# Performance work log

Measured on AMD Instinct MI355X. Metric: run time of the kernel, lower is better.

## Reference

```python
import jax, jax.numpy as jnp
import numpy as np

B, T, H = 2, 2048, 1024
NUM_HEADS = 16
HEAD_DIM = H // NUM_HEADS
MAX_REL = 4


def setup_inputs() -> dict:
    key = jax.random.key(0)
    ks = jax.random.split(key, 12)
    s = 1.0 / np.sqrt(H)
    inp = {
        "x": jax.random.normal(ks[0], (B, T, H), dtype=jnp.float32),
        "text_mask": jax.random.randint(ks[1], (B, T), 0, 2, dtype=jnp.int32),
        "Wq": jax.random.normal(ks[2], (H, H), dtype=jnp.float32) * s,
        "bq": jnp.zeros((H,), dtype=jnp.float32),
        "Wk": jax.random.normal(ks[3], (H, H), dtype=jnp.float32) * s,
        "bk": jnp.zeros((H,), dtype=jnp.float32),
        "Wv": jax.random.normal(ks[4], (H, H), dtype=jnp.float32) * s,
        "bv": jnp.zeros((H,), dtype=jnp.float32),
        "Wo": jax.random.normal(ks[5], (H, H), dtype=jnp.float32) * s,
        "bo": jnp.zeros((H,), dtype=jnp.float32),
        "rel_bias": jax.random.normal(ks[6], (2 * MAX_REL + 1, NUM_HEADS), dtype=jnp.float32),
    }
    return inp


def reference(x, text_mask, Wq, bq, Wk, bk, Wv, bv, Wo, bo, rel_bias):
    b, t, h = x.shape
    scale = HEAD_DIM ** (-0.5)

    def proj(W, bias):
        # [b,t,h] -> [b,heads,t,head_dim]
        return (x @ W.T + bias).reshape(b, t, NUM_HEADS, HEAD_DIM).transpose(0, 2, 1, 3)

    q = proj(Wq, bq)
    k = proj(Wk, bk)
    v = proj(Wv, bv)

    scores = jnp.einsum("bhqd,bhkd->bhqk", q, k) * scale  # [b,heads,t,t]

    pos = jnp.arange(t)
    rel = jnp.clip(pos[None, :] - pos[:, None], -MAX_REL, MAX_REL) + MAX_REL  # [t,t]
    bias = rel_bias[rel]  # [t,t,heads]
    scores = scores + bias.transpose(2, 0, 1)[None]  # broadcast over batch

    key_valid = text_mask.astype(bool)  # [b,t]
    scores = jnp.where(key_valid[:, None, None, :], scores, -10000.0)

    attn = jax.nn.softmax(scores, axis=-1)
    hidden = jnp.einsum("bhqk,bhkd->bhqd", attn, v)
    hidden = hidden.transpose(0, 2, 1, 3).reshape(b, t, h)
    out = hidden @ Wo.T + bo
    return out * text_mask.astype(out.dtype)[:, :, None]
```

## Files before the change

### kernel.cpp

```cpp
#include <hip/hip_runtime.h>
#include <hip/hip_bf16.h>

#define B_ 2
#define T_ 2048
#define H_ 1024
#define NH 16
#define HD 64

typedef __attribute__((ext_vector_type(8))) short bf16x8;
typedef __attribute__((ext_vector_type(4))) short bf16x4;
typedef __attribute__((ext_vector_type(4))) float f32x4;

#define ASYNC_COPY16(gptr, lptr)                                              \
    __builtin_amdgcn_global_load_lds(                                         \
        (const __attribute__((address_space(1))) void*)(gptr),                \
        (__attribute__((address_space(3))) void*)(lptr), 16, 0, 0)

#if __has_builtin(__builtin_amdgcn_exp2f)
#define EXP2(x) __builtin_amdgcn_exp2f(x)
#else
static __device__ inline float EXP2(float x) {
    float r;
    asm volatile("v_exp_f32 %0, %1" : "=v"(r) : "v"(x));
    return r;
}
#endif

static __device__ inline unsigned short f2bf(float f) {
    union { float f; unsigned u; } v; v.f = f;
    unsigned r = v.u + 0x7fff + ((v.u >> 16) & 1);
    return (unsigned short)(r >> 16);
}

static __device__ inline unsigned pkbf(float a, float b) {
    float2 t2; t2.x = a; t2.y = b;
    __hip_bfloat162 h = __float22bfloat162_rn(t2);
    union { __hip_bfloat162 h; unsigned u; } cv; cv.h = h;
    return cv.u;
}

static __device__ inline bf16x4 mk4(unsigned lo, unsigned hi) {
    union { bf16x4 v; unsigned u[2]; } cv;
    cv.u[0] = lo; cv.u[1] = hi;
    return cv.v;
}

static __device__ inline f32x4 zero4() {
    f32x4 z = {0.f, 0.f, 0.f, 0.f};
    return z;
}

#define LOG2E 1.44269504088896f

__global__ void cvt_kernel(const float* __restrict__ x,
                           const float* __restrict__ wq,
                           const float* __restrict__ wk,
                           const float* __restrict__ wv,
                           const float* __restrict__ wo,
                           const int* __restrict__ maskp,
                           unsigned short* __restrict__ dst,
                           unsigned* __restrict__ cidx,
                           unsigned short* __restrict__ vidx,
                           unsigned short* __restrict__ maskc,
                           unsigned* __restrict__ meta,
                           float* __restrict__ outz) {
    if (blockIdx.x > 8192) {
        long long idx =
            ((long long)(blockIdx.x - 8193) * 256 + threadIdx.x) * 4;
        if (idx < 4194304LL) {
            float4 z = {0.f, 0.f, 0.f, 0.f};
            *(float4*)(outz + idx) = z;
        }
        return;
    }
    if (blockIdx.x == 8192) {
        __shared__ unsigned ps[256];
        int t = threadIdx.x;
        int base = t * 16;
        int bb = base >> 11;
        unsigned mv = 0, cnt = 0;
#pragma unroll
        for (int i = 0; i < 16; i++) {
            if (maskp[base + i]) { mv |= (1u << i); cnt++; }
        }
        ps[t] = cnt;
        __syncthreads();
        for (int off = 1; off < 128; off <<= 1) {
            unsigned add = ((t & 127) >= off) ? ps[t - off] : 0;
            __syncthreads();
            ps[t] += add;
            __syncthreads();
        }
        unsigned cnt0 = ps[127], cnt1 = ps[255];
        unsigned ex = ps[t] - cnt;
        unsigned local = ex;
        unsigned g = (bb ? cnt0 : 0) + ex;
        for (int i = 0; i < 16; i++) {
            if (mv & (1u << i)) {
                cidx[g] = (unsigned)(base + i);
                vidx[bb * 2048 + local] =
                    (unsigned short)(base + i - bb * 2048);
                maskc[bb * 2048 + local] = 0x3F80;
                g++; local++;
            }
        }
        if (t == 0) { meta[0] = cnt0; meta[1] = cnt1; meta[2] = cnt0 + cnt1; }
        __syncthreads();
        unsigned C = cnt0 + cnt1;
        for (unsigned i = C + t; i < 4224; i += 256) cidx[i] = 0;
        for (unsigned i = cnt0 + t; i < 2048; i += 256) {
            vidx[i] = 0; maskc[i] = 0;
        }
        for (unsigned i = cnt1 + t; i < 2048; i += 256) {
            vidx[2048 + i] = 0; maskc[2048 + i] = 0;
        }
        return;
    }
    long long i0 = ((long long)blockIdx.x * blockDim.x + threadIdx.x) * 4;
    const float* src; long long off;
    if (i0 < 4194304LL)      { src = x;  off = i0; }
    else if (i0 < 5242880LL) { src = wq; off = i0 - 4194304LL; }
    else if (i0 < 6291456LL) { src = wk; off = i0 - 5242880LL; }
    else if (i0 < 7340032LL) { src = wv; off = i0 - 6291456LL; }
    else                     { src = wo; off = i0 - 7340032LL; }
    float4 f = *(const float4*)(src + off);
    ushort4 o;
    o.x = f2bf(f.x); o.y = f2bf(f.y); o.z = f2bf(f.z); o.w = f2bf(f.w);
    *(ushort4*)(dst + i0) = o;
}

__global__ __launch_bounds__(256) void qkv_gemm(
    const unsigned short* __restrict__ A,
    const unsigned short* __restrict__ Bm,
    const float* __restrict__ bq, const float* __restrict__ bk,
    const float* __restrict__ bv,
    const unsigned* __restrict__ cidx, const unsigned* __restrict__ meta,
    unsigned short* __restrict__ qout, unsigned short* __restrict__ kout,
    unsigned short* __restrict__ vout) {
    const int K = 1024;
    int C  = (int)meta[2];
    int c0 = (int)meta[0];
    int m0 = blockIdx.y * 64, n0 = blockIdx.x * 128;
    if (m0 >= C) return;
    __shared__ __align__(16) unsigned short As[64 * 32];
    __shared__ __align__(16) unsigned short Bs[128 * 32];
    int t = threadIdx.x;
    int w = t >> 6, lane = t & 63;
    int wm = (w >> 1) * 32, wn = (w & 1) * 64;
    int c = lane & 15, qd = lane >> 4;

    f32x4 acc[2][4];
#pragma unroll
    for (int i = 0; i < 2; i++)
#pragma unroll
        for (int j = 0; j < 4; j++) acc[i][j] = zero4();

    int srow = t >> 2, sseg = (t & 3) * 8;
    int r1 = (int)cidx[m0 + srow];
    const unsigned short* ag1 = A + (long long)r1 * K + sseg;
    const unsigned short* bg1 = Bm + (long long)(n0 + srow) * K + sseg;
    const unsigned short* bg2 = bg1 + 64LL * K;
    unsigned short* la1 = As + t * 8;
    unsigned short* lb1 = Bs + t * 8;
    unsigned short* lb2 = Bs + (t + 256) * 8;

    for (int kk = 0; kk < K; kk += 32) {
        __syncthreads();
        ASYNC_COPY16(ag1 + kk, la1);
        ASYNC_COPY16(bg1 + kk, lb1);
        ASYNC_COPY16(bg2 + kk, lb2);
        __syncthreads();
        bf16x8 af[2], bf[4];
#pragma unroll
        for (int i = 0; i < 2; i++)
            af[i] = *(const bf16x8*)(As + (wm + i * 16 + c) * 32 + qd * 8);
#pragma unroll
        for (int j = 0; j < 4; j++)
            bf[j] = *(const bf16x8*)(Bs + (wn + j * 16 + c) * 32 + qd * 8);
#pragma unroll
        for (int i = 0; i < 2; i++)
#pragma unroll
            for (int j = 0; j < 4; j++)
                acc[i][j] = __builtin_amdgcn_mfma_f32_16x16x32_bf16(
                    af[i], bf[j], acc[i][j], 0, 0, 0);
    }

    int gr[2][4];
#pragma unroll
    for (int i = 0; i < 2; i++)
#pragma unroll
        for (int r = 0; r < 4; r++) {
            int m = m0 + wm + i * 16 + qd * 4 + r;
            gr[i][r] = (m < C) ? (int)cidx[m] : -1;
        }

    const float QSCALE = 0.125f * LOG2E;
#pragma unroll
    for (int i = 0; i < 2; i++) {
        int m_base = m0 + wm + i * 16 + qd * 4;
#pragma unroll
        for (int j = 0; j < 4; j++) {
            int n = n0 + wn + j * 16 + c;
            int sel = n >> 10, within = n & 1023;
            int head = within >> 6, d = within & 63;
            if (sel == 0) {
                float ba = bq[within];
#pragma unroll
                for (int r = 0; r < 4; r++) {
                    if (gr[i][r] >= 0) {
                        int bb = gr[i][r] >> 11;
                        int loc = (m_base + r) - (bb ? c0 : 0);
                        qout[(((long long)(bb * NH + head)) * T_ + loc) * HD +
                             d] = f2bf((acc[i][j][r] + ba) * QSCALE);
                    }
                }
            } else if (sel == 1) {
                float ba = bk[within];
#pragma unroll
                for (int r = 0; r < 4; r++) {
                    if (gr[i][r] >= 0) {
                        int bb = gr[i][r] >> 11;
                        int loc = (m_base + r) - (bb ? c0 : 0);
                        kout[(((long long)(bb * NH + head)) * T_ + loc) * HD +
                             d] = f2bf(acc[i][j][r] + ba);
                    }
                }
            } else {
                float ba = bv[within];
                int g0 = gr[i][0], g3 = gr[i][3];
                int bb0 = g0 >> 11;
                int loc0 = m_base - (bb0 ? c0 : 0);
                if (g3 >= 0 && bb0 == (g3 >> 11) && ((loc0 & 3) == 0)) {
                    uint2 ov;
                    ov.x = pkbf(acc[i][j][0] + ba, acc[i][j][1] + ba);
                    ov.y = pkbf(acc[i][j][2] + ba, acc[i][j][3] + ba);
                    *(uint2*)(vout +
                              (((long long)(bb0 * NH + head)) * HD + d) * T_ +
                              loc0) = ov;
                } else {
#pragma unroll
                    for (int r = 0; r < 4; r++) {
                        if (gr[i][r] >= 0) {
                            int bb = gr[i][r] >> 11;
                            int loc = (m_base + r) - (bb ? c0 : 0);
                            vout[(((long long)(bb * NH + head)) * HD + d) *
                                     T_ +
                                 loc] = f2bf(acc[i][j][r] + ba);
                        }
                    }
                }
            }
        }
    }
}

__global__ __launch_bounds__(256) void out_gemm(
    const unsigned short* __restrict__ A,
    const unsigned short* __restrict__ Bm,
    const float* __restrict__ bo,
    const unsigned* __restrict__ cidx, const unsigned* __restrict__ meta,
    float* __restrict__ out) {
    const int K = 1024;
    int C = (int)meta[2];
    int m0 = blockIdx.y * 64, n0 = blockIdx.x * 64;
    if (m0 >= C) return;
    __shared__ __align__(16) unsigned short As[64 * 32];
    __shared__ __align__(16) unsigned short Bs[64 * 32];
    int t = threadIdx.x;
    int w = t >> 6, lane = t & 63;
    int wm = (w >> 1) * 32, wn = (w & 1) * 32;
    int c = lane & 15, qd = lane >> 4;

    f32x4 acc[2][2];
#pragma unroll
    for (int i = 0; i < 2; i++)
#pragma unroll
        for (int j = 0; j < 2; j++) acc[i][j] = zero4();

    int srow = t >> 2, sseg = (t & 3) * 8;
    int r1 = (int)cidx[m0 + srow];
    const unsigned short* ag1 = A + (long long)r1 * K + sseg;
    const unsigned short* bg1 = Bm + (long long)(n0 + srow) * K + sseg;
    unsigned short* la1 = As + t * 8;
    unsigned short* lb1 = Bs + t * 8;

    for (int kk = 0; kk < K; kk += 32) {
        __syncthreads();
        ASYNC_COPY16(ag1 + kk, la1);
        ASYNC_COPY16(bg1 + kk, lb1);
        __syncthreads();
        bf16x8 af[2], bf[2];
#pragma unroll
        for (int i = 0; i < 2; i++)
            af[i] = *(const bf16x8*)(As + (wm + i * 16 + c) * 32 + qd * 8);
#pragma unroll
        for (int j = 0; j < 2; j++)
            bf[j] = *(const bf16x8*)(Bs + (wn + j * 16 + c) * 32 + qd * 8);
#pragma unroll
        for (int i = 0; i < 2; i++)
#pragma unroll
            for (int j = 0; j < 2; j++)
                acc[i][j] = __builtin_amdgcn_mfma_f32_16x16x32_bf16(
                    af[i], bf[j], acc[i][j], 0, 0, 0);
    }

#pragma unroll
    for (int i = 0; i < 2; i++) {
#pragma unroll
        for (int r = 0; r < 4; r++) {
            int m = m0 + wm + i * 16 + qd * 4 + r;
            if (m < C) {
                long long g = (long long)cidx[m];
#pragma unroll
                for (int j = 0; j < 2; j++) {
                    int n = n0 + wn + j * 16 + c;
                    out[g * 1024 + n] = acc[i][j][r] + bo[n];
                }
            }
        }
    }
}

__global__ __launch_bounds__(256, 2) void attn_kernel(
    const unsigned short* __restrict__ qg,
    const unsigned short* __restrict__ kg,
    const unsigned short* __restrict__ vTg,
    const float* __restrict__ rel_bias,
    const unsigned short* __restrict__ maskc,
    const unsigned short* __restrict__ vidxg,
    const unsigned* __restrict__ meta,
    unsigned short* __restrict__ hid) {
    int hb = blockIdx.x, qt = blockIdx.y;
    int h = hb & 15, b = hb >> 4;
    int cnt = (int)meta[b];
    if (qt * 128 >= cnt) return;
    int nkt = (cnt + 63) >> 6;
    int t = threadIdx.x, w = t >> 6, lane = t & 63;
    int c = lane & 15, qd = lane >> 4;

    __shared__ __align__(16) unsigned short lk[2][64 * 72];
    __shared__ __align__(16) unsigned short lvT[2][64 * 72];
    __shared__ __align__(16) unsigned short lmk[2][64];
    __shared__ __align__(16) unsigned short lki[2][64];
    __shared__ float lrbf[16];

    if (t < 9) lrbf[t] = rel_bias[t * 16 + h] * LOG2E;
    float rb0 = rel_bias[0 * 16 + h] * LOG2E;
    float rb8 = rel_bias[8 * 16 + h] * LOG2E;

    const unsigned short* qp =
        qg + (((long long)(b * NH + h)) * T_ + qt * 128) * HD;
    const unsigned short* kp = kg + ((long long)(b * NH + h)) * T_ * HD;
    const unsigned short* vp = vTg + ((long long)(b * NH + h)) * HD * T_;

    bf16x8 qf[2][2];
#pragma unroll
    for (int mt = 0; mt < 2; mt++)
#pragma unroll
        for (int ks = 0; ks < 2; ks++)
            qf[mt][ks] = *(const bf16x8*)(qp + (w * 32 + mt * 16 + c) * HD +
                                          ks * 32 + qd * 8);

    const int imin = qt * 128 + w * 32;
    int imin_t = (int)vidxg[b * 2048 + min(imin, cnt - 1)];
    int imax_t = (int)vidxg[b * 2048 + min(imin + 31, cnt - 1)];
    int itrue[2];
#pragma unroll
    for (int mt = 0; mt < 2; mt++)
        itrue[mt] =
            (int)vidxg[b * 2048 + min(imin + mt * 16 + c, cnt - 1)];

    f32x4 o[4][2];
    f32x4 lacc[2];
#pragma unroll
    for (int dt = 0; dt < 4; dt++)
#pragma unroll
        for (int mt = 0; mt < 2; mt++) o[dt][mt] = zero4();
    lacc[0] = zero4(); lacc[1] = zero4();

    int srow = t >> 2, sseg = (t & 3) * 16;
    const unsigned short* kst = kp + srow * HD + sseg;
    const unsigned short* vst = vp + srow * T_ + sseg;
    const unsigned short* mst = maskc + b * 2048 + t;
    const unsigned short* ist = vidxg + b * 2048 + t * 8;

    uint4 rk0 = *(const uint4*)(kst);
    uint4 rk1 = *(const uint4*)(kst + 8);
    uint4 rv0 = *(const uint4*)(vst);
    uint4 rv1 = *(const uint4*)(vst + 8);
    unsigned short rm = (t < 64) ? *mst : 0;
    uint4 rki = {0, 0, 0, 0};
    if (t < 8) rki = *(const uint4*)(ist);

    for (int kt = 0; kt < nkt; kt++) {
        unsigned short* KB = lk[kt & 1];
        unsigned short* VB = lvT[kt & 1];
        unsigned short* MK = lmk[kt & 1];
        unsigned short* KI = lki[kt & 1];
        *(uint4*)(KB + srow * 72 + sseg)     = rk0;
        *(uint4*)(KB + srow * 72 + sseg + 8) = rk1;
        *(uint4*)(VB + srow * 72 + sseg)     = rv0;
        *(uint4*)(VB + srow * 72 + sseg + 8) = rv1;
        if (t < 64) MK[t] = rm;
        if (t < 8) *(uint4*)(KI + t * 8) = rki;
        {
            int ktn = (kt < nkt - 1) ? kt + 1 : nkt - 1;
            rk0 = *(const uint4*)(kst + ktn * 64 * HD);
            rk1 = *(const uint4*)(kst + ktn * 64 * HD + 8);
            rv0 = *(const uint4*)(vst + ktn * 64);
            rv1 = *(const uint4*)(vst + ktn * 64 + 8);
            if (t < 64) rm = mst[ktn * 64];
            if (t < 8) rki = *(const uint4*)(ist + ktn * 64);
        }
        __syncthreads();

        int j0 = kt * 64;
        int jlo_t = (int)KI[0];
        int jhi_t = (int)KI[min(63, cnt - 1 - j0)];
        bool far_lo = (jhi_t <= imin_t - 4);
        bool far_hi = (jlo_t >= imax_t + 4);
        float ub = far_lo ? rb0 : rb8;
        bool nearband = !(far_lo || far_hi);

#pragma unroll
        for (int jt = 0; jt < 4; jt++) {
            bf16x8 kf0 = *(const bf16x8*)(KB + (jt * 16 + c) * 72 + qd * 8);
            bf16x8 kf1 =
                *(const bf16x8*)(KB + (jt * 16 + c) * 72 + 32 + qd * 8);
            bf16x4 vld4 = *(const bf16x4*)(MK + jt * 16 + qd * 4);
            ushort4 kiv = *(const ushort4*)(KI + jt * 16 + qd * 4);
            bf16x4 vf[4];
#pragma unroll
            for (int dt = 0; dt < 4; dt++)
                vf[dt] = *(const bf16x4*)(VB + (dt * 16 + c) * 72 + jt * 16 +
                                          qd * 4);
#pragma unroll
            for (int mt = 0; mt < 2; mt++) {
                f32x4 acc = zero4();
                acc = __builtin_amdgcn_mfma_f32_16x16x32_bf16(kf0, qf[mt][0],
                                                              acc, 0, 0, 0);
                acc = __builtin_amdgcn_mfma_f32_16x16x32_bf16(kf1, qf[mt][1],
                                                              acc, 0, 0, 0);
                float p0, p1, p2, p3;
                if (nearband) {
                    int it = itrue[mt];
                    int r0 = (int)kiv.x - it;
                    r0 = r0 < -4 ? -4 : (r0 > 4 ? 4 : r0);
                    int r1 = (int)kiv.y - it;
                    r1 = r1 < -4 ? -4 : (r1 > 4 ? 4 : r1);
                    int r2 = (int)kiv.z - it;
                    r2 = r2 < -4 ? -4 : (r2 > 4 ? 4 : r2);
                    int r3 = (int)kiv.w - it;
                    r3 = r3 < -4 ? -4 : (r3 > 4 ? 4 : r3);
                    p0 = EXP2(acc[0] + lrbf[r0 + 4]);
                    p1 = EXP2(acc[1] + lrbf[r1 + 4]);
                    p2 = EXP2(acc[2] + lrbf[r2 + 4]);
                    p3 = EXP2(acc[3] + lrbf[r3 + 4]);
                } else {
                    p0 = EXP2(acc[0] + ub);
                    p1 = EXP2(acc[1] + ub);
                    p2 = EXP2(acc[2] + ub);
                    p3 = EXP2(acc[3] + ub);
                }
                bf16x4 pfrag = mk4(pkbf(p0, p1), pkbf(p2, p3));
                lacc[mt] = __builtin_amdgcn_mfma_f32_16x16x16bf16_1k(
                    vld4, pfrag, lacc[mt], 0, 0, 0);
#pragma unroll
                for (int dt = 0; dt < 4; dt++)
                    o[dt][mt] = __builtin_amdgcn_mfma_f32_16x16x16bf16_1k(
                        vf[dt], pfrag, o[dt][mt], 0, 0, 0);
            }
        }
    }

#pragma unroll
    for (int mt = 0; mt < 2; mt++) {
        int rc = imin + mt * 16 + c;
        if (rc < cnt) {
            float invl = 1.0f / lacc[mt][0];
            long long row = (long long)b * T_ + itrue[mt];
#pragma unroll
            for (int dt = 0; dt < 4; dt++) {
                uint2 ov;
                ov.x = pkbf(o[dt][mt][0] * invl, o[dt][mt][1] * invl);
                ov.y = pkbf(o[dt][mt][2] * invl, o[dt][mt][3] * invl);
                *(uint2*)(hid + row * H_ + h * HD + dt * 16 + qd * 4) = ov;
            }
        }
    }
}

extern "C" void kernel_launch(void* const* d_in, const int* in_sizes, int n_in,
                              void* d_out, int out_size, void* d_ws,
                              size_t ws_size, hipStream_t stream) {
    const float* x    = (const float*)d_in[0];
    const int* maskp  = (const int*)d_in[1];
    const float* Wq   = (const float*)d_in[2];
    const float* bq   = (const float*)d_in[3];
    const float* Wk   = (const float*)d_in[4];
    const float* bk   = (const float*)d_in[5];
    const float* Wv   = (const float*)d_in[6];
    const float* bv   = (const float*)d_in[7];
    const float* Wo   = (const float*)d_in[8];
    const float* bo   = (const float*)d_in[9];
    const float* rb   = (const float*)d_in[10];
    float* out        = (float*)d_out;

    unsigned short* ws = (unsigned short*)d_ws;
    unsigned short* xb    = ws;
    unsigned short* wqkv  = ws + 4194304LL;
    unsigned short* wo_b  = ws + 7340032LL;
    unsigned short* qb    = ws + 8388608LL;
    unsigned short* kb    = ws + 12582912LL;
    unsigned short* vTb   = ws + 16777216LL;
    unsigned short* hid   = ws + 20971520LL;
    unsigned* meta        = (unsigned*)(ws + 25165824LL);
    unsigned* cidx        = (unsigned*)(ws + 25165856LL);
    unsigned short* vidx  = ws + 25174304LL;
    unsigned short* maskc = ws + 25178400LL;

    cvt_kernel<<<12289, 256, 0, stream>>>(x, Wq, Wk, Wv, Wo, maskp, ws, cidx,
                                          vidx, maskc, meta, out);
    qkv_gemm<<<dim3(24, 64), 256, 0, stream>>>(xb, wqkv, bq, bk, bv, cidx,
                                               meta, qb, kb, vTb);
    attn_kernel<<<dim3(32, 16), 256, 0, stream>>>(qb, kb, vTb, rb, maskc,
                                                  vidx, meta, hid);
    out_gemm<<<dim3(16, 64), 256, 0, stream>>>(hid, wo_b, bo, cidx, meta,
                                               out);
}
```

Measured before the change: 181.9 us.

## Split attention key range across two wave groups per block and merge partials

Attention blocks grow to 512 threads split into two groups of four waves. Each group handles alternating 64-key tiles with its own double-buffered LDS, and the partial outputs and row sums are combined through LDS at the end. This doubles the waves working on each query tile, aiming for better latency hiding and occupancy on the compacted key loop. In exchange, LDS use per block doubles, each group refills its staging registers with an extra key tile (the clamped last one) that is never consumed, and the merge adds an extra reduction and barrier.

Result: no change. 185.0 us (+1.7%).

```diff
diff --git a/kernel.cpp b/kernel.cpp
--- a/kernel.cpp
+++ b/kernel.cpp
@@ -321,7 +321,7 @@
     }
 }
 
-__global__ __launch_bounds__(256, 2) void attn_kernel(
+__global__ __launch_bounds__(512, 2) void attn_kernel(
     const unsigned short* __restrict__ qg,
     const unsigned short* __restrict__ kg,
     const unsigned short* __restrict__ vTg,
@@ -335,13 +335,17 @@
     int cnt = (int)meta[b];
     if (qt * 128 >= cnt) return;
     int nkt = (cnt + 63) >> 6;
-    int t = threadIdx.x, w = t >> 6, lane = t & 63;
+    int t = threadIdx.x;
+    int g = t >> 8;
+    int tg = t & 255;
+    int w = tg >> 6;
+    int lane = t & 63;
     int c = lane & 15, qd = lane >> 4;
 
-    __shared__ __align__(16) unsigned short lk[2][64 * 72];
-    __shared__ __align__(16) unsigned short lvT[2][64 * 72];
-    __shared__ __align__(16) unsigned short lmk[2][64];
-    __shared__ __align__(16) unsigned short lki[2][64];
+    __shared__ __align__(16) unsigned short lk[2][2][64 * 72];
+    __shared__ __align__(16) unsigned short lvT[2][2][64 * 72];
+    __shared__ __align__(16) unsigned short lmk[2][2][64];
+    __shared__ __align__(16) unsigned short lki[2][2][64];
     __shared__ float lrbf[16];
 
     if (t < 9) lrbf[t] = rel_bias[t * 16 + h] * LOG2E;
@@ -378,43 +382,48 @@
         for (int mt = 0; mt < 2; mt++) o[dt][mt] = zero4();
     lacc[0] = zero4(); lacc[1] = zero4();
 
-    int srow = t >> 2, sseg = (t & 3) * 16;
+    int srow = tg >> 2, sseg = (tg & 3) * 16;
     const unsigned short* kst = kp + srow * HD + sseg;
     const unsigned short* vst = vp + srow * T_ + sseg;
-    const unsigned short* mst = maskc + b * 2048 + t;
-    const unsigned short* ist = vidxg + b * 2048 + t * 8;
-
-    uint4 rk0 = *(const uint4*)(kst);
-    uint4 rk1 = *(const uint4*)(kst + 8);
-    uint4 rv0 = *(const uint4*)(vst);
-    uint4 rv1 = *(const uint4*)(vst + 8);
-    unsigned short rm = (t < 64) ? *mst : 0;
+    const unsigned short* mst = maskc + b * 2048 + tg;
+    const unsigned short* ist = vidxg + b * 2048 + tg * 8;
+
+    int kt0 = min(g, nkt - 1);
+    uint4 rk0 = *(const uint4*)(kst + kt0 * 64 * HD);
+    uint4 rk1 = *(const uint4*)(kst + kt0 * 64 * HD + 8);
+    uint4 rv0 = *(const uint4*)(vst + kt0 * 64);
+    uint4 rv1 = *(const uint4*)(vst + kt0 * 64 + 8);
+    unsigned short rm = (tg < 64) ? mst[kt0 * 64] : 0;
     uint4 rki = {0, 0, 0, 0};
-    if (t < 8) rki = *(const uint4*)(ist);
-
-    for (int kt = 0; kt < nkt; kt++) {
-        unsigned short* KB = lk[kt & 1];
-        unsigned short* VB = lvT[kt & 1];
-        unsigned short* MK = lmk[kt & 1];
-        unsigned short* KI = lki[kt & 1];
+    if (tg < 8) rki = *(const uint4*)(ist + kt0 * 64);
+
+    int maxiter = (nkt + 1) >> 1;
+    for (int it = 0; it < maxiter; it++) {
+        int kta = g + 2 * it;
+        bool active = (kta < nkt);
+        unsigned short* KB = lk[g][it & 1];
+        unsigned short* VB = lvT[g][it & 1];
+        unsigned short* MK = lmk[g][it & 1];
+        unsigned short* KI = lki[g][it & 1];
         *(uint4*)(KB + srow * 72 + sseg)     = rk0;
         *(uint4*)(KB + srow * 72 + sseg + 8) = rk1;
         *(uint4*)(VB + srow * 72 + sseg)     = rv0;
         *(uint4*)(VB + srow * 72 + sseg + 8) = rv1;
-        if (t < 64) MK[t] = rm;
-        if (t < 8) *(uint4*)(KI + t * 8) = rki;
+        if (tg < 64) MK[tg] = rm;
+        if (tg < 8) *(uint4*)(KI + tg * 8) = rki;
         {
-            int ktn = (kt < nkt - 1) ? kt + 1 : nkt - 1;
+            int ktn = min(kta + 2, nkt - 1);
             rk0 = *(const uint4*)(kst + ktn * 64 * HD);
             rk1 = *(const uint4*)(kst + ktn * 64 * HD + 8);
             rv0 = *(const uint4*)(vst + ktn * 64);
             rv1 = *(const uint4*)(vst + ktn * 64 + 8);
-            if (t < 64) rm = mst[ktn * 64];
-            if (t < 8) rki = *(const uint4*)(ist + ktn * 64);
-        }
-        __syncthreads();
-
-        int j0 = kt * 64;
+            if (tg < 64) rm = mst[ktn * 64];
+            if (tg < 8) rki = *(const uint4*)(ist + ktn * 64);
+        }
+        __syncthreads();
+        if (!active) continue;
+
+        int j0 = kta * 64;
         int jlo_t = (int)KI[0];
         int jhi_t = (int)KI[min(63, cnt - 1 - j0)];
         bool far_lo = (jhi_t <= imin_t - 4);
@@ -443,14 +452,14 @@
                                                               acc, 0, 0, 0);
                 float p0, p1, p2, p3;
                 if (nearband) {
-                    int it = itrue[mt];
-                    int r0 = (int)kiv.x - it;
+                    int itq = itrue[mt];
+                    int r0 = (int)kiv.x - itq;
                     r0 = r0 < -4 ? -4 : (r0 > 4 ? 4 : r0);
-                    int r1 = (int)kiv.y - it;
+                    int r1 = (int)kiv.y - itq;
                     r1 = r1 < -4 ? -4 : (r1 > 4 ? 4 : r1);
-                    int r2 = (int)kiv.z - it;
+                    int r2 = (int)kiv.z - itq;
                     r2 = r2 < -4 ? -4 : (r2 > 4 ? 4 : r2);
-                    int r3 = (int)kiv.w - it;
+                    int r3 = (int)kiv.w - itq;
                     r3 = r3 < -4 ? -4 : (r3 > 4 ? 4 : r3);
                     p0 = EXP2(acc[0] + lrbf[r0 + 4]);
                     p1 = EXP2(acc[1] + lrbf[r1 + 4]);
@@ -473,18 +482,44 @@
         }
     }
 
-#pragma unroll
-    for (int mt = 0; mt < 2; mt++) {
-        int rc = imin + mt * 16 + c;
-        if (rc < cnt) {
-            float invl = 1.0f / lacc[mt][0];
-            long long row = (long long)b * T_ + itrue[mt];
-#pragma unroll
-            for (int dt = 0; dt < 4; dt++) {
-                uint2 ov;
-                ov.x = pkbf(o[dt][mt][0] * invl, o[dt][mt][1] * invl);
-                ov.y = pkbf(o[dt][mt][2] * invl, o[dt][mt][3] * invl);
-                *(uint2*)(hid + row * H_ + h * HD + dt * 16 + qd * 4) = ov;
+    __syncthreads();
+    float* cb = (float*)(&lk[0][0][0]);
+    int li = w * 64 + lane;
+    if (g == 1) {
+#pragma unroll
+        for (int dt = 0; dt < 4; dt++)
+#pragma unroll
+            for (int mt = 0; mt < 2; mt++)
+#pragma unroll
+                for (int r = 0; r < 4; r++)
+                    cb[li * 34 + dt * 8 + mt * 4 + r] = o[dt][mt][r];
+        cb[li * 34 + 32] = lacc[0][0];
+        cb[li * 34 + 33] = lacc[1][0];
+    }
+    __syncthreads();
+    if (g == 0) {
+#pragma unroll
+        for (int mt = 0; mt < 2; mt++) {
+            int rc = imin + mt * 16 + c;
+            if (rc < cnt) {
+                float lt = lacc[mt][0] + cb[li * 34 + 32 + mt];
+                float invl = 1.0f / lt;
+                long long row = (long long)b * T_ + itrue[mt];
+#pragma unroll
+                for (int dt = 0; dt < 4; dt++) {
+                    float o0 = o[dt][mt][0] + cb[li * 34 + dt * 8 + mt * 4];
+                    float o1 =
+                        o[dt][mt][1] + cb[li * 34 + dt * 8 + mt * 4 + 1];
+                    float o2 =
+                        o[dt][mt][2] + cb[li * 34 + dt * 8 + mt * 4 + 2];
+                    float o3 =
+                        o[dt][mt][3] + cb[li * 34 + dt * 8 + mt * 4 + 3];
+                    uint2 ov;
+                    ov.x = pkbf(o0 * invl, o1 * invl);
+                    ov.y = pkbf(o2 * invl, o3 * invl);
+                    *(uint2*)(hid + row * H_ + h * HD + dt * 16 + qd * 4) =
+                        ov;
+                }
             }
         }
     }
@@ -523,7 +558,7 @@
                                           vidx, maskc, meta, out);
     qkv_gemm<<<dim3(24, 64), 256, 0, stream>>>(xb, wqkv, bq, bk, bv, cidx,
                                                meta, qb, kb, vTb);
-    attn_kernel<<<dim3(32, 16), 256, 0, stream>>>(qb, kb, vTb, rb, maskc,
+    attn_kernel<<<dim3(32, 16), 512, 0, stream>>>(qb, kb, vTb, rb, maskc,
                                                   vidx, meta, hid);
     out_gemm<<<dim3(16, 64), 256, 0, stream>>>(hid, wo_b, bo, cidx, meta,
                                                out);
```

## Split attention over key range into two halves and combine partials

Applied to the files above, without the earlier changes.

Adds a grid z-dimension so each attention block processes half of the key tiles, writing unnormalized fp32 partial outputs and row sums to workspace. A new combine kernel sums the two partials, normalizes, and writes bf16 hidden rows at the original token positions. This aims to raise occupancy and parallelism on the attention stage, since the compacted sequence gives only a few hundred blocks. The cost is extra global traffic for fp32 partials and an additional kernel launch. It relies on softmax without a running max, which the code before already did.

After: 182.1 us. About the same (+0.1%).

```diff
diff --git a/kernel.cpp b/kernel.cpp
--- a/kernel.cpp
+++ b/kernel.cpp
@@ -329,12 +329,16 @@
     const unsigned short* __restrict__ maskc,
     const unsigned short* __restrict__ vidxg,
     const unsigned* __restrict__ meta,
-    unsigned short* __restrict__ hid) {
-    int hb = blockIdx.x, qt = blockIdx.y;
+    float* __restrict__ pO,
+    float* __restrict__ pl) {
+    int hb = blockIdx.x, qt = blockIdx.y, z = blockIdx.z;
     int h = hb & 15, b = hb >> 4;
     int cnt = (int)meta[b];
     if (qt * 128 >= cnt) return;
     int nkt = (cnt + 63) >> 6;
+    int nh2 = (nkt + 1) >> 1;
+    int ktbase = z ? nh2 : 0;
+    int myn = z ? (nkt - nh2) : nh2;
     int t = threadIdx.x, w = t >> 6, lane = t & 63;
     int c = lane & 15, qd = lane >> 4;
 
@@ -384,19 +388,21 @@
     const unsigned short* mst = maskc + b * 2048 + t;
     const unsigned short* ist = vidxg + b * 2048 + t * 8;
 
-    uint4 rk0 = *(const uint4*)(kst);
-    uint4 rk1 = *(const uint4*)(kst + 8);
-    uint4 rv0 = *(const uint4*)(vst);
-    uint4 rv1 = *(const uint4*)(vst + 8);
-    unsigned short rm = (t < 64) ? *mst : 0;
+    int kt0 = min(ktbase, nkt - 1);
+    uint4 rk0 = *(const uint4*)(kst + kt0 * 64 * HD);
+    uint4 rk1 = *(const uint4*)(kst + kt0 * 64 * HD + 8);
+    uint4 rv0 = *(const uint4*)(vst + kt0 * 64);
+    uint4 rv1 = *(const uint4*)(vst + kt0 * 64 + 8);
+    unsigned short rm = (t < 64) ? mst[kt0 * 64] : 0;
     uint4 rki = {0, 0, 0, 0};
-    if (t < 8) rki = *(const uint4*)(ist);
-
-    for (int kt = 0; kt < nkt; kt++) {
-        unsigned short* KB = lk[kt & 1];
-        unsigned short* VB = lvT[kt & 1];
-        unsigned short* MK = lmk[kt & 1];
-        unsigned short* KI = lki[kt & 1];
+    if (t < 8) rki = *(const uint4*)(ist + kt0 * 64);
+
+    for (int it = 0; it < myn; it++) {
+        int kta = ktbase + it;
+        unsigned short* KB = lk[it & 1];
+        unsigned short* VB = lvT[it & 1];
+        unsigned short* MK = lmk[it & 1];
+        unsigned short* KI = lki[it & 1];
         *(uint4*)(KB + srow * 72 + sseg)     = rk0;
         *(uint4*)(KB + srow * 72 + sseg + 8) = rk1;
         *(uint4*)(VB + srow * 72 + sseg)     = rv0;
@@ -404,7 +410,7 @@
         if (t < 64) MK[t] = rm;
         if (t < 8) *(uint4*)(KI + t * 8) = rki;
         {
-            int ktn = (kt < nkt - 1) ? kt + 1 : nkt - 1;
+            int ktn = min(kta + 1, ktbase + myn - 1);
             rk0 = *(const uint4*)(kst + ktn * 64 * HD);
             rk1 = *(const uint4*)(kst + ktn * 64 * HD + 8);
             rv0 = *(const uint4*)(vst + ktn * 64);
@@ -414,7 +420,7 @@
         }
         __syncthreads();
 
-        int j0 = kt * 64;
+        int j0 = kta * 64;
         int jlo_t = (int)KI[0];
         int jhi_t = (int)KI[min(63, cnt - 1 - j0)];
         bool far_lo = (jhi_t <= imin_t - 4);
@@ -443,14 +449,14 @@
                                                               acc, 0, 0, 0);
                 float p0, p1, p2, p3;
                 if (nearband) {
-                    int it = itrue[mt];
-                    int r0 = (int)kiv.x - it;
+                    int itq = itrue[mt];
+                    int r0 = (int)kiv.x - itq;
                     r0 = r0 < -4 ? -4 : (r0 > 4 ? 4 : r0);
-                    int r1 = (int)kiv.y - it;
+                    int r1 = (int)kiv.y - itq;
                     r1 = r1 < -4 ? -4 : (r1 > 4 ? 4 : r1);
-                    int r2 = (int)kiv.z - it;
+                    int r2 = (int)kiv.z - itq;
                     r2 = r2 < -4 ? -4 : (r2 > 4 ? 4 : r2);
-                    int r3 = (int)kiv.w - it;
+                    int r3 = (int)kiv.w - itq;
                     r3 = r3 < -4 ? -4 : (r3 > 4 ? 4 : r3);
                     p0 = EXP2(acc[0] + lrbf[r0 + 4]);
                     p1 = EXP2(acc[1] + lrbf[r1 + 4]);
@@ -473,20 +479,53 @@
         }
     }
 
+    float* po = pO + ((long long)(z * 32 + hb)) * 2048 * 64;
+    float* plz = pl + ((long long)(z * 32 + hb)) * 2048;
 #pragma unroll
     for (int mt = 0; mt < 2; mt++) {
-        int rc = imin + mt * 16 + c;
-        if (rc < cnt) {
-            float invl = 1.0f / lacc[mt][0];
-            long long row = (long long)b * T_ + itrue[mt];
-#pragma unroll
-            for (int dt = 0; dt < 4; dt++) {
-                uint2 ov;
-                ov.x = pkbf(o[dt][mt][0] * invl, o[dt][mt][1] * invl);
-                ov.y = pkbf(o[dt][mt][2] * invl, o[dt][mt][3] * invl);
-                *(uint2*)(hid + row * H_ + h * HD + dt * 16 + qd * 4) = ov;
-            }
-        }
+        int row = imin + mt * 16 + c;
+#pragma unroll
+        for (int dt = 0; dt < 4; dt++)
+            *(f32x4*)(po + (long long)row * 64 + dt * 16 + qd * 4) =
+                o[dt][mt];
+        if (qd == 0) plz[row] = lacc[mt][0];
+    }
+}
+
+__global__ __launch_bounds__(256) void combine_kernel(
+    const float* __restrict__ pO, const float* __restrict__ pl,
+    const unsigned short* __restrict__ vidxg,
+    const unsigned* __restrict__ meta,
+    unsigned short* __restrict__ hid) {
+    int hb = blockIdx.x, rb = blockIdx.y;
+    int b = hb >> 4, h = hb & 15;
+    int cnt = (int)meta[b];
+    int t = threadIdx.x;
+    int row = rb * 128 + (t >> 1);
+    if (row >= cnt) return;
+    int dh = (t & 1) * 32;
+    long long base = (((long long)hb) * 2048 + row) * 64 + dh;
+    const float* p0 = pO + base;
+    const float* p1 = pO + 4194304LL + base;
+    float l = pl[hb * 2048 + row] + pl[65536 + hb * 2048 + row];
+    float invl = 1.0f / l;
+    int trow = (int)vidxg[b * 2048 + row];
+    unsigned short* hp =
+        hid + ((long long)b * T_ + trow) * H_ + h * 64 + dh;
+    unsigned pk[16];
+#pragma unroll
+    for (int i = 0; i < 8; i++) {
+        float4 a = *(const float4*)(p0 + i * 4);
+        float4 c4 = *(const float4*)(p1 + i * 4);
+        pk[2 * i] = pkbf((a.x + c4.x) * invl, (a.y + c4.y) * invl);
+        pk[2 * i + 1] = pkbf((a.z + c4.z) * invl, (a.w + c4.w) * invl);
+    }
+#pragma unroll
+    for (int j = 0; j < 4; j++) {
+        uint4 ov;
+        ov.x = pk[4 * j]; ov.y = pk[4 * j + 1];
+        ov.z = pk[4 * j + 2]; ov.w = pk[4 * j + 3];
+        *(uint4*)(hp + j * 8) = ov;
     }
 }
 
@@ -518,13 +557,16 @@
     unsigned* cidx        = (unsigned*)(ws + 25165856LL);
     unsigned short* vidx  = ws + 25174304LL;
     unsigned short* maskc = ws + 25178400LL;
+    float* pO   = (float*)(ws + 26214400LL);
+    float* pl   = (float*)(ws + 26214400LL + 16777216LL);
 
     cvt_kernel<<<12289, 256, 0, stream>>>(x, Wq, Wk, Wv, Wo, maskp, ws, cidx,
                                           vidx, maskc, meta, out);
     qkv_gemm<<<dim3(24, 64), 256, 0, stream>>>(xb, wqkv, bq, bk, bv, cidx,
                                                meta, qb, kb, vTb);
-    attn_kernel<<<dim3(32, 16), 256, 0, stream>>>(qb, kb, vTb, rb, maskc,
-                                                  vidx, meta, hid);
+    attn_kernel<<<dim3(32, 16, 2), 256, 0, stream>>>(qb, kb, vTb, rb, maskc,
+                                                     vidx, meta, pO, pl);
+    combine_kernel<<<dim3(32, 16), 256, 0, stream>>>(pO, pl, vidx, meta, hid);
     out_gemm<<<dim3(16, 64), 256, 0, stream>>>(hid, wo_b, bo, cidx, meta,
                                                out);
 }
```
